# Kernel tuning notes

Measured on AMD Instinct MI355X. Metric: run time of the kernel, lower is better.

The kernel has to match this reference:

```python
import jax, jax.numpy as jnp
import numpy as np

B = 16384; T = 12; MLP = 1024; ZD = 32; H = 128; NSG = 4
N_STATE = 6; NPRED = 2; DT = 0.4 * 4


def _linear_init(k, out_d, in_d):
    s = 1.0 / np.sqrt(in_d)
    kw, kb = jax.random.split(k)
    W = jax.random.uniform(kw, (out_d, in_d), minval=-s, maxval=s, dtype=jnp.float32)
    b = jax.random.uniform(kb, (out_d,), minval=-s, maxval=s, dtype=jnp.float32)
    return W, b


def setup_inputs() -> dict:
    key = jax.random.key(0)
    ks = jax.random.split(key, 16)
    W_dec_hidden, b_dec_hidden = _linear_init(ks[0], H, MLP + ZD)
    W_to_vel, b_to_vel = _linear_init(ks[1], NPRED, N_STATE)
    W_ih, b_ih = _linear_init(ks[2], 3 * H, MLP + ZD + 2 * NPRED)
    W_hh, b_hh = _linear_init(ks[3], 3 * H, H)
    W_mu, b_mu = _linear_init(ks[4], NPRED, H)
    W_std, b_std = _linear_init(ks[5], NPRED, H)
    W_sg, b_sg = _linear_init(ks[6], NPRED, 4)
    return {
        'last_obs_st': jax.random.normal(ks[7], (B, N_STATE), dtype=jnp.float32),
        'last_obs_pos': jax.random.normal(ks[8], (B, 2), dtype=jnp.float32),
        'enc_h_feat': jax.random.normal(ks[9], (B, MLP), dtype=jnp.float32),
        'z': jax.random.normal(ks[10], (B, ZD), dtype=jnp.float32),
        'sg': jax.random.normal(ks[11], (B, NSG, 2), dtype=jnp.float32),
        'fut_traj': jax.random.normal(ks[12], (T, B, N_STATE), dtype=jnp.float32),
        'sg_update_idx': jnp.array([0, 3, 7, 11], dtype=jnp.int32),
        'W_dec_hidden': W_dec_hidden, 'b_dec_hidden': b_dec_hidden,
        'W_to_vel': W_to_vel, 'b_to_vel': b_to_vel,
        'W_ih': W_ih, 'b_ih': b_ih, 'W_hh': W_hh, 'b_hh': b_hh,
        'W_mu': W_mu, 'b_mu': b_mu, 'W_std': W_std, 'b_std': b_std,
        'W_sg': W_sg, 'b_sg': b_sg,
    }


def reference(last_obs_st, last_obs_pos, enc_h_feat, z, sg, fut_traj, sg_update_idx,
              W_dec_hidden, b_dec_hidden, W_to_vel, b_to_vel, W_ih, b_ih,
              W_hh, b_hh, W_mu, b_mu, W_std, b_std, W_sg, b_sg):
    upd = np.asarray(sg_update_idx)  # static control-flow schedule
    zx = jnp.concatenate([enc_h_feat, z], axis=1)              # [B, MLP+ZD]
    h0 = zx @ W_dec_hidden.T + b_dec_hidden                    # [B, H]
    a0 = last_obs_st @ W_to_vel.T + b_to_vel                   # [B, 2]

    pts = jnp.concatenate([last_obs_pos[:, None], sg], axis=1)  # [B, 1+NSG, 2]
    pts = (pts - pts[:, :1]) / 100.0
    v = (pts[:, 1:] - pts[:, :-1]) / DT                         # [B, NSG, 2]
    sg_state = jnp.concatenate([pts[:, 1:], v], axis=-1)        # [B, NSG, 4]
    sg_feat_upd = jnp.einsum('bjf,of->jbo', sg_state, W_sg) + b_sg  # [NSG, B, 2]

    # sg_feat held constant between update steps (matches python-loop gating)
    j_idx = np.clip(np.searchsorted(upd, np.arange(T), side='right') - 1, 0, len(upd) - 1)
    sg_feat_all = sg_feat_upd[j_idx]                            # [T, B, 2]

    # teacher forcing: a for step i>0 is fut_traj[i-1,:,2:4]
    a_seq = jnp.concatenate([a0[None], fut_traj[:-1, :, 2:4]], axis=0)  # [T, B, 2]

    # precompute input-side GRU gate projections (zx part is step-invariant)
    D = zx.shape[1]
    gates_zx = zx @ W_ih[:, :D].T                               # [B, 3H]
    gates_a = jnp.einsum('tbi,gi->tbg', a_seq, W_ih[:, D:D + 2])
    gates_sg = jnp.einsum('tbi,gi->tbg', sg_feat_all, W_ih[:, D + 2:])
    gates_x = gates_zx[None] + gates_a + gates_sg + b_ih        # [T, B, 3H]

    def step(h, gx):
        gh = h @ W_hh.T + b_hh
        r = jax.nn.sigmoid(gx[:, :H] + gh[:, :H])
        zg = jax.nn.sigmoid(gx[:, H:2 * H] + gh[:, H:2 * H])
        n = jnp.tanh(gx[:, 2 * H:] + r * gh[:, 2 * H:])
        h_new = (1.0 - zg) * n + zg * h
        mu = h_new @ W_mu.T + b_mu
        std = jnp.sqrt(jnp.exp(h_new @ W_std.T + b_std))
        return h_new, (mu, std)

    _, (mus, stds) = jax.lax.scan(step, h0, gates_x)
    return mus, stds  # each [T, B, 2] — params of returned Normal
```

## Files before the change

### kernel.cpp

```cpp
#include <hip/hip_runtime.h>
#include <hip/hip_bf16.h>

#define BN 16384
#define TT 12
#define MLP 1024
#define ZD 32
#define HD 128
#define KD 1056
#define GN 384
#define WIH_LD 1060
#define NSG 4
#define DTC 1.6f
#define PLD 512
#define SLD 40

typedef __attribute__((ext_vector_type(8))) short short8;
typedef __attribute__((ext_vector_type(4))) short short4_t;
typedef __attribute__((ext_vector_type(4))) float floatx4;
typedef __hip_bfloat16 bf16;

__device__ __forceinline__ float bf2f(bf16 v) { return __bfloat162float(v); }
__device__ __forceinline__ bf16 f2bf(float v) { return __float2bfloat16(v); }
__device__ __forceinline__ short bfbits(float x) {
    bf16 t = __float2bfloat16(x);
    return __builtin_bit_cast(short, t);
}
__device__ __forceinline__ float bfraw2f(unsigned short u) {
    return __uint_as_float(((unsigned int)u) << 16);
}
__device__ __forceinline__ float sigm(float x) {
    return __builtin_amdgcn_rcpf(1.0f + __expf(-x));
}
__device__ __forceinline__ float tanh_f(float x) {
    return 1.0f - 2.0f * __builtin_amdgcn_rcpf(1.0f + __expf(2.0f * x));
}
__device__ __forceinline__ short8 pack8(floatx4 a, floatx4 b) {
    short8 v;
    v[0]=bfbits(a[0]); v[1]=bfbits(a[1]); v[2]=bfbits(a[2]); v[3]=bfbits(a[3]);
    v[4]=bfbits(b[0]); v[5]=bfbits(b[1]); v[6]=bfbits(b[2]); v[7]=bfbits(b[3]);
    return v;
}
__device__ __forceinline__ short8 ld8f(const float* q) {
    return pack8(*(const floatx4*)q, *(const floatx4*)(q + 4));
}
__device__ __forceinline__ void barrier_lgkm() {
    asm volatile("s_waitcnt lgkmcnt(0)\n\ts_barrier" ::: "memory");
}

struct GP {
    const float *lst, *lpos, *enc, *zz, *sg, *fut;
    const int* upd;
    const float *Wdec, *bdec, *Wtv, *btv, *Wih, *bih, *Whh, *bhh;
    const float *Wmu, *bmu, *Wstd, *bstd, *Wsg, *bsg;
    const bf16* P;
    float* out;
};

__global__ __launch_bounds__(512, 4) void k_gemm(
    const float* __restrict__ enc, const float* __restrict__ zz,
    const float* __restrict__ Wih, const float* __restrict__ Wdec,
    bf16* __restrict__ P)
{
    __shared__ __align__(16) bf16 sA[2][128 * SLD];
    __shared__ __align__(16) bf16 sB[2][128 * SLD];
    const int tid = threadIdx.x;
    const int lane = tid & 63;
    const int wav = tid >> 6;
    const int wm2 = wav >> 2;
    const int wn2 = wav & 3;
    const int c = lane & 15;
    const int quad = lane >> 4;
    const int m0 = blockIdx.x * 128;
    const int n0 = blockIdx.y * 128;

    const int srow = tid >> 2;
    const int scq = (tid & 3) * 8;
    const int nn = n0 + srow;
    const float* arow = enc + (size_t)(m0 + srow) * MLP + scq;
    const float* zrow = zz + (size_t)(m0 + srow) * ZD + scq;
    const float* brow = (nn < GN) ? Wih + (size_t)nn * WIH_LD + scq
                                  : Wdec + (size_t)(nn - GN) * KD + scq;

    floatx4 pa[2][2], pb[2][2];
#pragma unroll
    for (int s0 = 0; s0 < 2; s0++) {
        const float* qa = arow + s0 * 32;
        const float* qb = brow + s0 * 32;
        pa[s0][0] = *(const floatx4*)qa; pa[s0][1] = *(const floatx4*)(qa + 4);
        pb[s0][0] = *(const floatx4*)qb; pb[s0][1] = *(const floatx4*)(qb + 4);
    }

    floatx4 acc[4][2];
#pragma unroll
    for (int i = 0; i < 4; i++)
#pragma unroll
        for (int j = 0; j < 2; j++) acc[i][j] = floatx4{0.f, 0.f, 0.f, 0.f};

    for (int kc = 0; kc < 33; kc++) {
        const int sl = kc & 1;
        *(short8*)&sA[sl][srow * SLD + scq] = pack8(pa[sl][0], pa[sl][1]);
        *(short8*)&sB[sl][srow * SLD + scq] = pack8(pb[sl][0], pb[sl][1]);
        if (kc + 2 < 33) {
            const int k2 = (kc + 2) * 32;
            const float* qa = (kc + 2 < 32) ? arow + k2 : zrow;
            const float* qb = brow + k2;
            pa[sl][0] = *(const floatx4*)qa; pa[sl][1] = *(const floatx4*)(qa + 4);
            pb[sl][0] = *(const floatx4*)qb; pb[sl][1] = *(const floatx4*)(qb + 4);
        }
        barrier_lgkm();
        short8 a[4], b[2];
#pragma unroll
        for (int i = 0; i < 4; i++)
            a[i] = *(const short8*)&sA[sl][(wm2 * 64 + i * 16 + c) * SLD + quad * 8];
#pragma unroll
        for (int j = 0; j < 2; j++)
            b[j] = *(const short8*)&sB[sl][(wn2 * 32 + j * 16 + c) * SLD + quad * 8];
#pragma unroll
        for (int i = 0; i < 4; i++)
#pragma unroll
            for (int j = 0; j < 2; j++)
                acc[i][j] = __builtin_amdgcn_mfma_f32_16x16x32_bf16(
                    a[i], b[j], acc[i][j], 0, 0, 0);
    }
#pragma unroll
    for (int i = 0; i < 4; i++)
#pragma unroll
        for (int j = 0; j < 2; j++)
#pragma unroll
            for (int r = 0; r < 4; r++)
                P[(size_t)(m0 + wm2 * 64 + i * 16 + quad * 4 + r) * PLD
                  + n0 + wn2 * 32 + j * 16 + c] = f2bf(acc[i][j][r]);
}

template<int FUSED> struct SMem {
    static constexpr int PRE_N = FUSED ? 32 * 512 : 16;
    bf16 pre[PRE_N];
    bf16 h[2][32][136];
    bf16 ext[TT][32][4];
    float sgf[NSG][32][2];
    float a0[32][2];
    float muw[4][132];
    float b4[4];
};

template<int FUSED>
__device__ __forceinline__ void heads_out(const SMem<FUSED>& s, const GP& p,
                                          int rows0, int t, int buf, int tid) {
    const int row = tid >> 2;
    const int sel = tid & 3;
    float sum = 0.0f;
#pragma unroll
    for (int k8 = 0; k8 < 16; k8++) {
        short8 hv = *(const short8*)(&s.h[buf][row][k8 * 8]);
#pragma unroll
        for (int u = 0; u < 8; u++)
            sum += bfraw2f((unsigned short)hv[u]) * s.muw[sel][k8 * 8 + u];
    }
    sum += s.b4[sel];
    const size_t TB2 = (size_t)TT * BN * 2;
    const size_t grow = (size_t)rows0 + row;
    if (sel < 2) p.out[((size_t)t * BN + grow) * 2 + sel] = sum;
    else p.out[TB2 + ((size_t)t * BN + grow) * 2 + (sel - 2)] = __expf(0.5f * sum);
}

template<int FUSED>
__global__ __launch_bounds__(512, 2) void k_gru(GP p) {
    __shared__ __align__(16) SMem<FUSED> s;
    const int tid = threadIdx.x;
    const int lane = tid & 63;
    const int wav = tid >> 6;
    const int wn = wav & 3;
    const int wm = wav >> 2;
    const int c = lane & 15;
    const int quad = lane >> 4;
    const int rows0 = blockIdx.x * 32;
    const int jb = wn * 32;

    if constexpr (FUSED) {
        floatx4 acc2[2][4];
#pragma unroll
        for (int i = 0; i < 2; i++)
#pragma unroll
            for (int j = 0; j < 4; j++) acc2[i][j] = floatx4{0.f, 0.f, 0.f, 0.f};
        const int nb = wav * 64;
        for (int kc = 0; kc < 33; kc++) {
            const int k = kc * 32 + quad * 8;
            short8 af[2], bf8[4];
            if (kc < 32) {
                af[0] = ld8f(p.enc + (size_t)(rows0 + c) * MLP + k);
                af[1] = ld8f(p.enc + (size_t)(rows0 + 16 + c) * MLP + k);
            } else {
                af[0] = ld8f(p.zz + (size_t)(rows0 + c) * ZD + (k - MLP));
                af[1] = ld8f(p.zz + (size_t)(rows0 + 16 + c) * ZD + (k - MLP));
            }
#pragma unroll
            for (int j = 0; j < 4; j++) {
                const int n = nb + j * 16 + c;
                bf8[j] = (n < GN) ? ld8f(p.Wih + (size_t)n * WIH_LD + k)
                                  : ld8f(p.Wdec + (size_t)(n - GN) * KD + k);
            }
#pragma unroll
            for (int i = 0; i < 2; i++)
#pragma unroll
                for (int j = 0; j < 4; j++)
                    acc2[i][j] = __builtin_amdgcn_mfma_f32_16x16x32_bf16(
                        af[i], bf8[j], acc2[i][j], 0, 0, 0);
        }
#pragma unroll
        for (int i = 0; i < 2; i++)
#pragma unroll
            for (int j = 0; j < 4; j++)
#pragma unroll
                for (int r = 0; r < 4; r++)
                    s.pre[(i * 16 + quad * 4 + r) * 512 + nb + j * 16 + c] =
                        f2bf(acc2[i][j][r]);
    }

    {
        int sel = tid >> 7, k = tid & 127;
        s.muw[sel][k] = (sel < 2) ? p.Wmu[sel * 128 + k] : p.Wstd[(sel - 2) * 128 + k];
    }
    if (tid < 4) s.b4[tid] = (tid < 2) ? p.bmu[tid] : p.bstd[tid - 2];
    if (tid < 32) {
        const int row = rows0 + tid;
        for (int pp = 0; pp < 2; pp++) {
            float sum = p.btv[pp];
            for (int f = 0; f < 6; f++)
                sum += p.lst[(size_t)row * 6 + f] * p.Wtv[pp * 6 + f];
            s.a0[tid][pp] = sum;
        }
        float px = p.lpos[(size_t)row * 2];
        float py = p.lpos[(size_t)row * 2 + 1];
        float prevx = 0.f, prevy = 0.f;
        for (int j = 0; j < NSG; j++) {
            float rx = (p.sg[((size_t)row * NSG + j) * 2] - px) * 0.01f;
            float ry = (p.sg[((size_t)row * NSG + j) * 2 + 1] - py) * 0.01f;
            float vx = (rx - prevx) * (1.0f / DTC), vy = (ry - prevy) * (1.0f / DTC);
            prevx = rx; prevy = ry;
            float st4[4] = {rx, ry, vx, vy};
            for (int pp = 0; pp < 2; pp++) {
                float sum = p.bsg[pp];
                for (int f = 0; f < 4; f++) sum += st4[f] * p.Wsg[pp * 4 + f];
                s.sgf[j][tid][pp] = sum;
            }
        }
    }
    int upd[4];
#pragma unroll
    for (int i = 0; i < 4; i++) upd[i] = p.upd[i];

    short8 Wb[2][3][4];
    short8 Wb4[2][2];
    float Wa2[2][2], Ws2[2][2], bhh2[2];
#pragma unroll
    for (int jt2 = 0; jt2 < 2; jt2++) {
#pragma unroll
        for (int g = 0; g < 3; g++) {
            const int n = g * 128 + jb + jt2 * 16 + c;
#pragma unroll
            for (int kc = 0; kc < 4; kc++)
                Wb[jt2][g][kc] = ld8f(p.Whh + (size_t)n * HD + kc * 32 + quad * 8);
            if (g < 2) {
                short8 v = {0, 0, 0, 0, 0, 0, 0, 0};
                if (quad == 0) {
                    const float* q = p.Wih + (size_t)n * WIH_LD + KD;
                    v[0] = bfbits(q[0]); v[1] = bfbits(q[1]);
                    v[2] = bfbits(q[2]); v[3] = bfbits(q[3]);
                }
                Wb4[jt2][g] = v;
            }
        }
        const int n2 = 256 + jb + jt2 * 16 + c;
        const float* q2 = p.Wih + (size_t)n2 * WIH_LD + KD;
        Wa2[jt2][0] = q2[0]; Wa2[jt2][1] = q2[1];
        Ws2[jt2][0] = q2[2]; Ws2[jt2][1] = q2[3];
        bhh2[jt2] = p.bhh[n2];
    }

    __syncthreads();

    floatx4 gzx[2][3];
#pragma unroll
    for (int jt2 = 0; jt2 < 2; jt2++) {
#pragma unroll
        for (int g = 0; g < 3; g++) {
            const int n = g * 128 + jb + jt2 * 16 + c;
            float bias = p.bih[n] + ((g < 2) ? p.bhh[n] : 0.0f);
            floatx4 v;
#pragma unroll
            for (int r = 0; r < 4; r++) {
                const int mrow = wm * 16 + quad * 4 + r;
                float raw;
                if constexpr (FUSED) raw = bf2f(s.pre[mrow * 512 + n]);
                else raw = bf2f(p.P[(size_t)(rows0 + mrow) * PLD + n]);
                v[r] = raw + bias;
            }
            gzx[jt2][g] = v;
        }
    }
    float hreg[2][4];
#pragma unroll
    for (int jt2 = 0; jt2 < 2; jt2++) {
        const int hcol = jb + jt2 * 16 + c;
        float bd = p.bdec[hcol];
#pragma unroll
        for (int r = 0; r < 4; r++) {
            const int mrow = wm * 16 + quad * 4 + r;
            float raw;
            if constexpr (FUSED) raw = bf2f(s.pre[mrow * 512 + GN + hcol]);
            else raw = bf2f(p.P[(size_t)(rows0 + mrow) * PLD + GN + hcol]);
            float hv = raw + bd;
            hreg[jt2][r] = hv;
            s.h[1][mrow][hcol] = f2bf(hv);
        }
    }
    if (tid < TT * 32) {
        const int t = tid >> 5, row = tid & 31;
        float a0v, a1v;
        if (t == 0) { a0v = s.a0[row][0]; a1v = s.a0[row][1]; }
        else {
            const float* fp = p.fut + ((size_t)(t - 1) * BN + rows0 + row) * 6 + 2;
            a0v = fp[0]; a1v = fp[1];
        }
        int jj = 0;
#pragma unroll
        for (int q = 1; q < NSG; q++) if (upd[q] <= t) jj = q;
        s.ext[t][row][0] = f2bf(a0v);
        s.ext[t][row][1] = f2bf(a1v);
        s.ext[t][row][2] = f2bf(s.sgf[jj][row][0]);
        s.ext[t][row][3] = f2bf(s.sgf[jj][row][1]);
    }
    __syncthreads();

    for (int t = 0; t < TT; t++) {
        const int bi = (t & 1) ^ 1;
        const int bo = t & 1;

        floatx4 acc[2][3];
#pragma unroll
        for (int jt2 = 0; jt2 < 2; jt2++) {
            acc[jt2][0] = gzx[jt2][0];
            acc[jt2][1] = gzx[jt2][1];
            floatx4 bb; bb[0] = bb[1] = bb[2] = bb[3] = bhh2[jt2];
            acc[jt2][2] = bb;
        }
#pragma unroll
        for (int kc = 0; kc < 4; kc++) {
            short8 am = *(const short8*)(&s.h[bi][wm * 16 + c][kc * 32 + quad * 8]);
#pragma unroll
            for (int jt2 = 0; jt2 < 2; jt2++)
#pragma unroll
                for (int g = 0; g < 3; g++)
                    acc[jt2][g] = __builtin_amdgcn_mfma_f32_16x16x32_bf16(
                        am, Wb[jt2][g][kc], acc[jt2][g], 0, 0, 0);
        }
        {
            short8 am4 = {0, 0, 0, 0, 0, 0, 0, 0};
            if (quad == 0) {
                short4_t e = *(const short4_t*)(&s.ext[t][wm * 16 + c][0]);
                am4[0] = e[0]; am4[1] = e[1]; am4[2] = e[2]; am4[3] = e[3];
            }
#pragma unroll
            for (int jt2 = 0; jt2 < 2; jt2++)
#pragma unroll
                for (int g = 0; g < 2; g++)
                    acc[jt2][g] = __builtin_amdgcn_mfma_f32_16x16x32_bf16(
                        am4, Wb4[jt2][g], acc[jt2][g], 0, 0, 0);
        }

        if (t > 0 && tid < 128) heads_out<FUSED>(s, p, rows0, t - 1, bi, tid);

#pragma unroll
        for (int r = 0; r < 4; r++) {
            const int mrow = wm * 16 + quad * 4 + r;
            short4_t e4 = *(const short4_t*)(&s.ext[t][mrow][0]);
            float a0v = bfraw2f((unsigned short)e4[0]);
            float a1v = bfraw2f((unsigned short)e4[1]);
            float s0v = bfraw2f((unsigned short)e4[2]);
            float s1v = bfraw2f((unsigned short)e4[3]);
#pragma unroll
            for (int jt2 = 0; jt2 < 2; jt2++) {
                float rr = sigm(acc[jt2][0][r]);
                float zg = sigm(acc[jt2][1][r]);
                float tn = a0v * Wa2[jt2][0] + a1v * Wa2[jt2][1]
                         + s0v * Ws2[jt2][0] + s1v * Ws2[jt2][1];
                float narg = gzx[jt2][2][r] + tn + rr * acc[jt2][2][r];
                float nn = tanh_f(narg);
                float hv = nn + zg * (hreg[jt2][r] - nn);
                hreg[jt2][r] = hv;
                s.h[bo][mrow][jb + jt2 * 16 + c] = f2bf(hv);
            }
        }
        barrier_lgkm();
    }
    if (tid < 128) heads_out<FUSED>(s, p, rows0, TT - 1, (TT - 1) & 1, tid);
}

extern "C" void kernel_launch(void* const* d_in, const int* in_sizes, int n_in,
                              void* d_out, int out_size, void* d_ws, size_t ws_size,
                              hipStream_t stream) {
    GP p;
    p.lst  = (const float*)d_in[0];
    p.lpos = (const float*)d_in[1];
    p.enc  = (const float*)d_in[2];
    p.zz   = (const float*)d_in[3];
    p.sg   = (const float*)d_in[4];
    p.fut  = (const float*)d_in[5];
    p.upd  = (const int*)d_in[6];
    p.Wdec = (const float*)d_in[7];
    p.bdec = (const float*)d_in[8];
    p.Wtv  = (const float*)d_in[9];
    p.btv  = (const float*)d_in[10];
    p.Wih  = (const float*)d_in[11];
    p.bih  = (const float*)d_in[12];
    p.Whh  = (const float*)d_in[13];
    p.bhh  = (const float*)d_in[14];
    p.Wmu  = (const float*)d_in[15];
    p.bmu  = (const float*)d_in[16];
    p.Wstd = (const float*)d_in[17];
    p.bstd = (const float*)d_in[18];
    p.Wsg  = (const float*)d_in[19];
    p.bsg  = (const float*)d_in[20];
    p.out  = (float*)d_out;
    p.P    = nullptr;

    const size_t needP = (size_t)BN * PLD * sizeof(bf16);
    if (ws_size >= needP) {
        bf16* P = (bf16*)d_ws;
        p.P = P;
        k_gemm<<<dim3(128, 4), 512, 0, stream>>>(p.enc, p.zz, p.Wih, p.Wdec, P);
        k_gru<0><<<512, 512, 0, stream>>>(p);
    } else {
        k_gru<1><<<512, 512, 0, stream>>>(p);
    }
}
```

Before: 263.0 us.

## Shrink GRU blocks to 16 rows and 256 threads, doubling grid size

Each GRU block now handles 16 batch rows with 4 waves instead of 32 rows with 8 waves, so the grid goes from 512 to 1024 blocks and launch bounds change to 256 threads with 4 blocks per CU. The goal is better occupancy and load balance across the mi355x CUs for the latency-bound recurrent loop, and less shared memory per block. In exchange, each block loads the full W_hh fragments for only half as many rows, and the fused GEMM path has each wave compute 8 column tiles over a single row tile.

```diff
diff --git a/kernel.cpp b/kernel.cpp
--- a/kernel.cpp
+++ b/kernel.cpp
@@ -13,6 +13,7 @@
 #define DTC 1.6f
 #define PLD 512
 #define SLD 40
+#define GRU_ROWS 16
 
 typedef __attribute__((ext_vector_type(8))) short short8;
 typedef __attribute__((ext_vector_type(4))) short short4_t;
@@ -133,12 +134,12 @@
 }
 
 template<int FUSED> struct SMem {
-    static constexpr int PRE_N = FUSED ? 32 * 512 : 16;
+    static constexpr int PRE_N = FUSED ? GRU_ROWS * 512 : 16;
     bf16 pre[PRE_N];
-    bf16 h[2][32][136];
-    bf16 ext[TT][32][4];
-    float sgf[NSG][32][2];
-    float a0[32][2];
+    bf16 h[2][GRU_ROWS][136];
+    bf16 ext[TT][GRU_ROWS][4];
+    float sgf[NSG][GRU_ROWS][2];
+    float a0[GRU_ROWS][2];
     float muw[4][132];
     float b4[4];
 };
@@ -164,64 +165,52 @@
 }
 
 template<int FUSED>
-__global__ __launch_bounds__(512, 2) void k_gru(GP p) {
+__global__ __launch_bounds__(256, 4) void k_gru(GP p) {
     __shared__ __align__(16) SMem<FUSED> s;
     const int tid = threadIdx.x;
     const int lane = tid & 63;
     const int wav = tid >> 6;
-    const int wn = wav & 3;
-    const int wm = wav >> 2;
+    const int wn = wav;
     const int c = lane & 15;
     const int quad = lane >> 4;
-    const int rows0 = blockIdx.x * 32;
+    const int rows0 = blockIdx.x * GRU_ROWS;
     const int jb = wn * 32;
 
     if constexpr (FUSED) {
-        floatx4 acc2[2][4];
-#pragma unroll
-        for (int i = 0; i < 2; i++)
-#pragma unroll
-            for (int j = 0; j < 4; j++) acc2[i][j] = floatx4{0.f, 0.f, 0.f, 0.f};
-        const int nb = wav * 64;
+        floatx4 acc2[8];
+#pragma unroll
+        for (int j = 0; j < 8; j++) acc2[j] = floatx4{0.f, 0.f, 0.f, 0.f};
+        const int nb = wav * 128;
         for (int kc = 0; kc < 33; kc++) {
             const int k = kc * 32 + quad * 8;
-            short8 af[2], bf8[4];
-            if (kc < 32) {
-                af[0] = ld8f(p.enc + (size_t)(rows0 + c) * MLP + k);
-                af[1] = ld8f(p.enc + (size_t)(rows0 + 16 + c) * MLP + k);
-            } else {
-                af[0] = ld8f(p.zz + (size_t)(rows0 + c) * ZD + (k - MLP));
-                af[1] = ld8f(p.zz + (size_t)(rows0 + 16 + c) * ZD + (k - MLP));
-            }
-#pragma unroll
-            for (int j = 0; j < 4; j++) {
+            short8 af, bf8[8];
+            if (kc < 32) af = ld8f(p.enc + (size_t)(rows0 + c) * MLP + k);
+            else         af = ld8f(p.zz + (size_t)(rows0 + c) * ZD + (k - MLP));
+#pragma unroll
+            for (int j = 0; j < 8; j++) {
                 const int n = nb + j * 16 + c;
                 bf8[j] = (n < GN) ? ld8f(p.Wih + (size_t)n * WIH_LD + k)
                                   : ld8f(p.Wdec + (size_t)(n - GN) * KD + k);
             }
 #pragma unroll
-            for (int i = 0; i < 2; i++)
-#pragma unroll
-                for (int j = 0; j < 4; j++)
-                    acc2[i][j] = __builtin_amdgcn_mfma_f32_16x16x32_bf16(
-                        af[i], bf8[j], acc2[i][j], 0, 0, 0);
-        }
-#pragma unroll
-        for (int i = 0; i < 2; i++)
-#pragma unroll
-            for (int j = 0; j < 4; j++)
-#pragma unroll
-                for (int r = 0; r < 4; r++)
-                    s.pre[(i * 16 + quad * 4 + r) * 512 + nb + j * 16 + c] =
-                        f2bf(acc2[i][j][r]);
-    }
-
-    {
-        int sel = tid >> 7, k = tid & 127;
+            for (int j = 0; j < 8; j++)
+                acc2[j] = __builtin_amdgcn_mfma_f32_16x16x32_bf16(
+                    af, bf8[j], acc2[j], 0, 0, 0);
+        }
+#pragma unroll
+        for (int j = 0; j < 8; j++)
+#pragma unroll
+            for (int r = 0; r < 4; r++)
+                s.pre[(quad * 4 + r) * 512 + nb + j * 16 + c] = f2bf(acc2[j][r]);
+    }
+
+#pragma unroll
+    for (int u = tid; u < 512; u += 256) {
+        int sel = u >> 7, k = u & 127;
         s.muw[sel][k] = (sel < 2) ? p.Wmu[sel * 128 + k] : p.Wstd[(sel - 2) * 128 + k];
     }
     if (tid < 4) s.b4[tid] = (tid < 2) ? p.bmu[tid] : p.bstd[tid - 2];
-    if (tid < 32) {
+    if (tid < GRU_ROWS) {
         const int row = rows0 + tid;
         for (int pp = 0; pp < 2; pp++) {
             float sum = p.btv[pp];
@@ -289,7 +278,7 @@
             floatx4 v;
 #pragma unroll
             for (int r = 0; r < 4; r++) {
-                const int mrow = wm * 16 + quad * 4 + r;
+                const int mrow = quad * 4 + r;
                 float raw;
                 if constexpr (FUSED) raw = bf2f(s.pre[mrow * 512 + n]);
                 else raw = bf2f(p.P[(size_t)(rows0 + mrow) * PLD + n]);
@@ -305,7 +294,7 @@
         float bd = p.bdec[hcol];
 #pragma unroll
         for (int r = 0; r < 4; r++) {
-            const int mrow = wm * 16 + quad * 4 + r;
+            const int mrow = quad * 4 + r;
             float raw;
             if constexpr (FUSED) raw = bf2f(s.pre[mrow * 512 + GN + hcol]);
             else raw = bf2f(p.P[(size_t)(rows0 + mrow) * PLD + GN + hcol]);
@@ -314,8 +303,8 @@
             s.h[1][mrow][hcol] = f2bf(hv);
         }
     }
-    if (tid < TT * 32) {
-        const int t = tid >> 5, row = tid & 31;
+    if (tid < TT * GRU_ROWS) {
+        const int t = tid >> 4, row = tid & (GRU_ROWS - 1);
         float a0v, a1v;
         if (t == 0) { a0v = s.a0[row][0]; a1v = s.a0[row][1]; }
         else {
@@ -346,7 +335,7 @@
         }
 #pragma unroll
         for (int kc = 0; kc < 4; kc++) {
-            short8 am = *(const short8*)(&s.h[bi][wm * 16 + c][kc * 32 + quad * 8]);
+            short8 am = *(const short8*)(&s.h[bi][c][kc * 32 + quad * 8]);
 #pragma unroll
             for (int jt2 = 0; jt2 < 2; jt2++)
 #pragma unroll
@@ -357,7 +346,7 @@
         {
             short8 am4 = {0, 0, 0, 0, 0, 0, 0, 0};
             if (quad == 0) {
-                short4_t e = *(const short4_t*)(&s.ext[t][wm * 16 + c][0]);
+                short4_t e = *(const short4_t*)(&s.ext[t][c][0]);
                 am4[0] = e[0]; am4[1] = e[1]; am4[2] = e[2]; am4[3] = e[3];
             }
 #pragma unroll
@@ -368,11 +357,11 @@
                         am4, Wb4[jt2][g], acc[jt2][g], 0, 0, 0);
         }
 
-        if (t > 0 && tid < 128) heads_out<FUSED>(s, p, rows0, t - 1, bi, tid);
+        if (t > 0 && tid < 64) heads_out<FUSED>(s, p, rows0, t - 1, bi, tid);
 
 #pragma unroll
         for (int r = 0; r < 4; r++) {
-            const int mrow = wm * 16 + quad * 4 + r;
+            const int mrow = quad * 4 + r;
             short4_t e4 = *(const short4_t*)(&s.ext[t][mrow][0]);
             float a0v = bfraw2f((unsigned short)e4[0]);
             float a1v = bfraw2f((unsigned short)e4[1]);
@@ -393,7 +382,7 @@
         }
         barrier_lgkm();
     }
-    if (tid < 128) heads_out<FUSED>(s, p, rows0, TT - 1, (TT - 1) & 1, tid);
+    if (tid < 64) heads_out<FUSED>(s, p, rows0, TT - 1, (TT - 1) & 1, tid);
 }
 
 extern "C" void kernel_launch(void* const* d_in, const int* in_sizes, int n_in,
@@ -429,8 +418,8 @@
         bf16* P = (bf16*)d_ws;
         p.P = P;
         k_gemm<<<dim3(128, 4), 512, 0, stream>>>(p.enc, p.zz, p.Wih, p.Wdec, P);
-        k_gru<0><<<512, 512, 0, stream>>>(p);
+        k_gru<0><<<BN / GRU_ROWS, 256, 0, stream>>>(p);
     } else {
-        k_gru<1><<<512, 512, 0, stream>>>(p);
-    }
-}
+        k_gru<1><<<BN / GRU_ROWS, 256, 0, stream>>>(p);
+    }
+}
```

After: 459.4 us. +74.7%, slower.

## Drop separate input GEMM kernel and always run fused GRU kernel

Applied to the files above, without the earlier changes.

Removes the standalone tiled k_gemm that wrote the input-gate and hidden-init projections to a bf16 workspace. The single fused k_gru, which computes the projection per 32-row block into shared memory before the recurrence, now always runs. This removes one launch and the workspace write and read-back. In exchange, the projection runs inside the GRU kernel with direct global loads and no LDS tiling, and the kernel needs more shared memory, which may reduce occupancy.

```diff
diff --git a/kernel.cpp b/kernel.cpp
--- a/kernel.cpp
+++ b/kernel.cpp
@@ -11,8 +11,6 @@
 #define WIH_LD 1060
 #define NSG 4
 #define DTC 1.6f
-#define PLD 512
-#define SLD 40
 
 typedef __attribute__((ext_vector_type(8))) short short8;
 typedef __attribute__((ext_vector_type(4))) short short4_t;
@@ -52,89 +50,11 @@
     const int* upd;
     const float *Wdec, *bdec, *Wtv, *btv, *Wih, *bih, *Whh, *bhh;
     const float *Wmu, *bmu, *Wstd, *bstd, *Wsg, *bsg;
-    const bf16* P;
     float* out;
 };
 
-__global__ __launch_bounds__(512, 4) void k_gemm(
-    const float* __restrict__ enc, const float* __restrict__ zz,
-    const float* __restrict__ Wih, const float* __restrict__ Wdec,
-    bf16* __restrict__ P)
-{
-    __shared__ __align__(16) bf16 sA[2][128 * SLD];
-    __shared__ __align__(16) bf16 sB[2][128 * SLD];
-    const int tid = threadIdx.x;
-    const int lane = tid & 63;
-    const int wav = tid >> 6;
-    const int wm2 = wav >> 2;
-    const int wn2 = wav & 3;
-    const int c = lane & 15;
-    const int quad = lane >> 4;
-    const int m0 = blockIdx.x * 128;
-    const int n0 = blockIdx.y * 128;
-
-    const int srow = tid >> 2;
-    const int scq = (tid & 3) * 8;
-    const int nn = n0 + srow;
-    const float* arow = enc + (size_t)(m0 + srow) * MLP + scq;
-    const float* zrow = zz + (size_t)(m0 + srow) * ZD + scq;
-    const float* brow = (nn < GN) ? Wih + (size_t)nn * WIH_LD + scq
-                                  : Wdec + (size_t)(nn - GN) * KD + scq;
-
-    floatx4 pa[2][2], pb[2][2];
-#pragma unroll
-    for (int s0 = 0; s0 < 2; s0++) {
-        const float* qa = arow + s0 * 32;
-        const float* qb = brow + s0 * 32;
-        pa[s0][0] = *(const floatx4*)qa; pa[s0][1] = *(const floatx4*)(qa + 4);
-        pb[s0][0] = *(const floatx4*)qb; pb[s0][1] = *(const floatx4*)(qb + 4);
-    }
-
-    floatx4 acc[4][2];
-#pragma unroll
-    for (int i = 0; i < 4; i++)
-#pragma unroll
-        for (int j = 0; j < 2; j++) acc[i][j] = floatx4{0.f, 0.f, 0.f, 0.f};
-
-    for (int kc = 0; kc < 33; kc++) {
-        const int sl = kc & 1;
-        *(short8*)&sA[sl][srow * SLD + scq] = pack8(pa[sl][0], pa[sl][1]);
-        *(short8*)&sB[sl][srow * SLD + scq] = pack8(pb[sl][0], pb[sl][1]);
-        if (kc + 2 < 33) {
-            const int k2 = (kc + 2) * 32;
-            const float* qa = (kc + 2 < 32) ? arow + k2 : zrow;
-            const float* qb = brow + k2;
-            pa[sl][0] = *(const floatx4*)qa; pa[sl][1] = *(const floatx4*)(qa + 4);
-            pb[sl][0] = *(const floatx4*)qb; pb[sl][1] = *(const floatx4*)(qb + 4);
-        }
-        barrier_lgkm();
-        short8 a[4], b[2];
-#pragma unroll
-        for (int i = 0; i < 4; i++)
-            a[i] = *(const short8*)&sA[sl][(wm2 * 64 + i * 16 + c) * SLD + quad * 8];
-#pragma unroll
-        for (int j = 0; j < 2; j++)
-            b[j] = *(const short8*)&sB[sl][(wn2 * 32 + j * 16 + c) * SLD + quad * 8];
-#pragma unroll
-        for (int i = 0; i < 4; i++)
-#pragma unroll
-            for (int j = 0; j < 2; j++)
-                acc[i][j] = __builtin_amdgcn_mfma_f32_16x16x32_bf16(
-                    a[i], b[j], acc[i][j], 0, 0, 0);
-    }
-#pragma unroll
-    for (int i = 0; i < 4; i++)
-#pragma unroll
-        for (int j = 0; j < 2; j++)
-#pragma unroll
-            for (int r = 0; r < 4; r++)
-                P[(size_t)(m0 + wm2 * 64 + i * 16 + quad * 4 + r) * PLD
-                  + n0 + wn2 * 32 + j * 16 + c] = f2bf(acc[i][j][r]);
-}
-
-template<int FUSED> struct SMem {
-    static constexpr int PRE_N = FUSED ? 32 * 512 : 16;
-    bf16 pre[PRE_N];
+struct SMem {
+    bf16 pre[32 * 512];
     bf16 h[2][32][136];
     bf16 ext[TT][32][4];
     float sgf[NSG][32][2];
@@ -143,8 +63,7 @@
     float b4[4];
 };
 
-template<int FUSED>
-__device__ __forceinline__ void heads_out(const SMem<FUSED>& s, const GP& p,
+__device__ __forceinline__ void heads_out(const SMem& s, const GP& p,
                                           int rows0, int t, int buf, int tid) {
     const int row = tid >> 2;
     const int sel = tid & 3;
@@ -163,9 +82,8 @@
     else p.out[TB2 + ((size_t)t * BN + grow) * 2 + (sel - 2)] = __expf(0.5f * sum);
 }
 
-template<int FUSED>
 __global__ __launch_bounds__(512, 2) void k_gru(GP p) {
-    __shared__ __align__(16) SMem<FUSED> s;
+    __shared__ __align__(16) SMem s;
     const int tid = threadIdx.x;
     const int lane = tid & 63;
     const int wav = tid >> 6;
@@ -176,7 +94,7 @@
     const int rows0 = blockIdx.x * 32;
     const int jb = wn * 32;
 
-    if constexpr (FUSED) {
+    {
         floatx4 acc2[2][4];
 #pragma unroll
         for (int i = 0; i < 2; i++)
@@ -290,10 +208,7 @@
 #pragma unroll
             for (int r = 0; r < 4; r++) {
                 const int mrow = wm * 16 + quad * 4 + r;
-                float raw;
-                if constexpr (FUSED) raw = bf2f(s.pre[mrow * 512 + n]);
-                else raw = bf2f(p.P[(size_t)(rows0 + mrow) * PLD + n]);
-                v[r] = raw + bias;
+                v[r] = bf2f(s.pre[mrow * 512 + n]) + bias;
             }
             gzx[jt2][g] = v;
         }
@@ -306,10 +221,7 @@
 #pragma unroll
         for (int r = 0; r < 4; r++) {
             const int mrow = wm * 16 + quad * 4 + r;
-            float raw;
-            if constexpr (FUSED) raw = bf2f(s.pre[mrow * 512 + GN + hcol]);
-            else raw = bf2f(p.P[(size_t)(rows0 + mrow) * PLD + GN + hcol]);
-            float hv = raw + bd;
+            float hv = bf2f(s.pre[mrow * 512 + GN + hcol]) + bd;
             hreg[jt2][r] = hv;
             s.h[1][mrow][hcol] = f2bf(hv);
         }
@@ -368,7 +280,7 @@
                         am4, Wb4[jt2][g], acc[jt2][g], 0, 0, 0);
         }
 
-        if (t > 0 && tid < 128) heads_out<FUSED>(s, p, rows0, t - 1, bi, tid);
+        if (t > 0 && tid < 128) heads_out(s, p, rows0, t - 1, bi, tid);
 
 #pragma unroll
         for (int r = 0; r < 4; r++) {
@@ -393,7 +305,7 @@
         }
         barrier_lgkm();
     }
-    if (tid < 128) heads_out<FUSED>(s, p, rows0, TT - 1, (TT - 1) & 1, tid);
+    if (tid < 128) heads_out(s, p, rows0, TT - 1, (TT - 1) & 1, tid);
 }
 
 extern "C" void kernel_launch(void* const* d_in, const int* in_sizes, int n_in,
@@ -422,15 +334,6 @@
     p.Wsg  = (const float*)d_in[19];
     p.bsg  = (const float*)d_in[20];
     p.out  = (float*)d_out;
-    p.P    = nullptr;
-
-    const size_t needP = (size_t)BN * PLD * sizeof(bf16);
-    if (ws_size >= needP) {
-        bf16* P = (bf16*)d_ws;
-        p.P = P;
-        k_gemm<<<dim3(128, 4), 512, 0, stream>>>(p.enc, p.zz, p.Wih, p.Wdec, P);
-        k_gru<0><<<512, 512, 0, stream>>>(p);
-    } else {
-        k_gru<1><<<512, 512, 0, stream>>>(p);
-    }
-}
+
+    k_gru<<<BN / 32, 512, 0, stream>>>(p);
+}
```

Measured after the change: 346.3 us. +31.6%, slower.
